# Performance work log

Hardware: AMD Instinct MI355X
Metric: run time of the kernel (lower is better)

## Reference

```python
import jax, jax.numpy as jnp
import numpy as np

EPS = 1e-12

def _natural_vvg_sym(x):
    """Natural vector visibility graph for one example.
    x: [S, D]. Returns symmetric 0/1 adjacency [S, S] = vg + vg.T (vg upper-triangular).
    Node a sees node b (a<b) iff for all a<c<b:
        y_c < y_b + (y_a - y_b) * (b - c) / (b - a),  y_k = <x_k, x_b> / ||x_b||
    """
    S = x.shape[0]
    t = jnp.arange(S, dtype=x.dtype)
    norms = jnp.maximum(jnp.linalg.norm(x, axis=-1), EPS)        # [S]
    Y = (x @ x.T) / norms[:, None]                                # Y[b,c] = <x_c,x_b>/||x_b||
    d = jnp.diagonal(Y)                                           # y_b = ||x_b||, [S]
    ta = t[:, None, None]   # a axis
    tb = t[None, :, None]   # b axis
    tc = t[None, None, :]   # c axis
    denom = jnp.where(tb != ta, tb - ta, jnp.ones((), x.dtype))   # avoid 0/0 on diagonal
    # visibility line at time c for pair (a,b): [S,S,S] indexed [a,b,c]
    line = d[None, :, None] + (Y.T[:, :, None] - d[None, :, None]) * (tb - tc) / denom
    between = (tc > ta) & (tc < tb)                               # strict interior points
    blocked = jnp.any((Y[None, :, :] >= line) & between, axis=-1) # [a,b]
    upper = t[None, :] > t[:, None]                               # b > a
    vg = (upper & ~blocked).astype(x.dtype)                       # upper-triangular adjacency
    return vg + vg.T


def setup_inputs() -> dict:
    key = jax.random.key(0)
    k1, k2 = jax.random.split(key)
    token_embs = jax.random.normal(k1, (8, 256, 768), dtype=jnp.float32)
    W = jax.random.normal(k2, (768, 4), dtype=jnp.float32)
    return {"token_embs": token_embs, "W": W}


def reference(token_embs, W):
    # vg_sym: [B, S, S]
    vg_sym = jax.vmap(_natural_vvg_sym)(token_embs)
    # torch: out[i] = multi_dot([vg, example, W])[0] == vg_sym[0] @ example @ W
    row0 = vg_sym[:, 0, :]                          # [B, S]
    h = jnp.einsum('bs,bsd->bd', row0, token_embs)  # [B, 768]
    logits = h @ W                                  # [B, n_class]
    return jax.nn.log_softmax(logits, axis=-1)
```

## Files before the change

kernel.cpp:

```cpp
#include <hip/hip_runtime.h>
#include <hip/hip_bf16.h>

constexpr int S  = 256;
constexpr int D  = 768;
constexpr int KQ = 8;
constexpr int KS = D / KQ;
constexpr int GROWS = KQ * S;

typedef _Float16 half8  __attribute__((ext_vector_type(8)));
typedef _Float16 half4v __attribute__((ext_vector_type(4)));
typedef float    f32x4  __attribute__((ext_vector_type(4)));

__device__ const int TI_MAP[10] = {0,1,1,2,2,2,3,3,3,3};
__device__ const int TJ_MAP[10] = {0,0,1,0,1,2,0,1,2,3};

__global__ __launch_bounds__(256) void gram_kernel(const float* __restrict__ X,
                                                   float* __restrict__ G) {
    const int ti    = TI_MAP[blockIdx.x];
    const int tj    = TJ_MAP[blockIdx.x];
    const int batch = blockIdx.y;
    const int kq    = blockIdx.z;

    const float* Xq = X + (size_t)batch * S * D + kq * KS;

    __shared__ _Float16 Ah[64][104], Al[64][104], Bh[64][104], Bl[64][104];

    const int t    = threadIdx.x;
    const int srow = t >> 2;
    const int sk   = (t & 3) * 24;

    const float* pa = Xq + (size_t)(ti * 64 + srow) * D + sk;
    const float* pb = Xq + (size_t)(tj * 64 + srow) * D + sk;

#pragma unroll
    for (int c = 0; c < 6; ++c) {
        const int ko = sk + c * 4;
        const float4 va = *(const float4*)(pa + c * 4);
        const float4 vb = *(const float4*)(pb + c * 4);
        half4v ha, la, hb, lb;
        ha.x = (_Float16)va.x; la.x = (_Float16)(va.x - (float)ha.x);
        ha.y = (_Float16)va.y; la.y = (_Float16)(va.y - (float)ha.y);
        ha.z = (_Float16)va.z; la.z = (_Float16)(va.z - (float)ha.z);
        ha.w = (_Float16)va.w; la.w = (_Float16)(va.w - (float)ha.w);
        hb.x = (_Float16)vb.x; lb.x = (_Float16)(vb.x - (float)hb.x);
        hb.y = (_Float16)vb.y; lb.y = (_Float16)(vb.y - (float)hb.y);
        hb.z = (_Float16)vb.z; lb.z = (_Float16)(vb.z - (float)hb.z);
        hb.w = (_Float16)vb.w; lb.w = (_Float16)(vb.w - (float)hb.w);
        *(half4v*)&Ah[srow][ko] = ha;
        *(half4v*)&Al[srow][ko] = la;
        *(half4v*)&Bh[srow][ko] = hb;
        *(half4v*)&Bl[srow][ko] = lb;
    }
    __syncthreads();

    const int lane = t & 63;
    const int w    = t >> 6;
    const int frow = lane & 15;
    const int fko  = (lane >> 4) * 8;

    f32x4 acc[4] = {};
#pragma unroll
    for (int ks = 0; ks < 3; ++ks) {
        const int k0 = ks * 32 + fko;
        const half8 ah = *(const half8*)&Ah[w * 16 + frow][k0];
        const half8 al = *(const half8*)&Al[w * 16 + frow][k0];
#pragma unroll
        for (int n = 0; n < 4; ++n) {
            const half8 bh = *(const half8*)&Bh[n * 16 + frow][k0];
            const half8 bl = *(const half8*)&Bl[n * 16 + frow][k0];
            acc[n] = __builtin_amdgcn_mfma_f32_16x16x32_f16(ah, bh, acc[n], 0, 0, 0);
            acc[n] = __builtin_amdgcn_mfma_f32_16x16x32_f16(ah, bl, acc[n], 0, 0, 0);
            acc[n] = __builtin_amdgcn_mfma_f32_16x16x32_f16(al, bh, acc[n], 0, 0, 0);
        }
    }

    float* gout = G + ((size_t)(batch * S + ti * 64 + w * 16 + (lane >> 4) * 4) * KQ + kq) * S
                    + tj * 64 + frow;
#pragma unroll
    for (int n = 0; n < 4; ++n)
#pragma unroll
        for (int r = 0; r < 4; ++r)
            gout[(size_t)r * GROWS + n * 16] = acc[n][r];
}

__global__ __launch_bounds__(256) void visxw_kernel(const float* __restrict__ X,
                                                    const float* __restrict__ Wm,
                                                    const float* __restrict__ G,
                                                    float* __restrict__ P,
                                                    float* __restrict__ wv) {
    const int batch = blockIdx.y;
    const int wave  = threadIdx.x >> 6;
    const int lane  = threadIdx.x & 63;
    const int b     = blockIdx.x * 4 + wave;

    const float* rbp = G + (size_t)(batch * S + b) * GROWS + 4 * lane;
    float4 s0 = make_float4(0.f, 0.f, 0.f, 0.f), s1 = s0, s2 = s0, s3 = s0;
    if (4 * lane <= b) {
#pragma unroll
        for (int sl = 0; sl < 2; ++sl) {
            const float4 v0 = *(const float4*)(rbp + (size_t)(4 * sl + 0) * S);
            const float4 v1 = *(const float4*)(rbp + (size_t)(4 * sl + 1) * S);
            const float4 v2 = *(const float4*)(rbp + (size_t)(4 * sl + 2) * S);
            const float4 v3 = *(const float4*)(rbp + (size_t)(4 * sl + 3) * S);
            s0.x += v0.x; s0.y += v0.y; s0.z += v0.z; s0.w += v0.w;
            s1.x += v1.x; s1.y += v1.y; s1.z += v1.z; s1.w += v1.w;
            s2.x += v2.x; s2.y += v2.y; s2.z += v2.z; s2.w += v2.w;
            s3.x += v3.x; s3.y += v3.y; s3.z += v3.z; s3.w += v3.w;
        }
    }
    float4 gs;
    gs.x = (s0.x + s1.x) + (s2.x + s3.x);
    gs.y = (s0.y + s1.y) + (s2.y + s3.y);
    gs.z = (s0.z + s1.z) + (s2.z + s3.z);
    gs.w = (s0.w + s1.w) + (s2.w + s3.w);

    const int bq = b & 3;
    float sel = (bq == 0) ? gs.x : ((bq == 1) ? gs.y : ((bq == 2) ? gs.z : gs.w));
    const float gb = __shfl(sel, b >> 2);
    const float g0 = __shfl(gs.x, 0);
    const float denom = (b > 0) ? (float)b : 1.0f;

    bool blocked = false;
    {
        const int c0 = 4 * lane;
#define VTEST(Q, GV) { const int c = c0 + (Q); \
        const float line = gb + ((g0 - gb) * (float)(b - c)) / denom; \
        if (c >= 1 && c < b && (GV) >= line) blocked = true; }
        VTEST(0, gs.x) VTEST(1, gs.y) VTEST(2, gs.z) VTEST(3, gs.w)
#undef VTEST
    }
    const bool visflag = (b >= 1) && !__any(blocked);

    const float* xs = X + ((size_t)batch * S + b) * D;
    float a0 = 0.f, a1 = 0.f, a2 = 0.f, a3 = 0.f;
#pragma unroll
    for (int i = 0; i < 3; ++i) {
        const int d0 = (lane + 64 * i) * 4;
        const float4 xv = *(const float4*)(xs + d0);
        const float xf[4] = {xv.x, xv.y, xv.z, xv.w};
#pragma unroll
        for (int j = 0; j < 4; ++j) {
            const float4 wq = *(const float4*)(Wm + (size_t)(d0 + j) * 4);
            a0 = fmaf(xf[j], wq.x, a0);
            a1 = fmaf(xf[j], wq.y, a1);
            a2 = fmaf(xf[j], wq.z, a2);
            a3 = fmaf(xf[j], wq.w, a3);
        }
    }
#pragma unroll
    for (int off = 32; off; off >>= 1) {
        a0 += __shfl_xor(a0, off);
        a1 += __shfl_xor(a1, off);
        a2 += __shfl_xor(a2, off);
        a3 += __shfl_xor(a3, off);
    }
    if (lane == 0) {
        float4 o = {a0, a1, a2, a3};
        *(float4*)(P + ((size_t)batch * S + b) * 4) = o;
        wv[batch * S + b] = visflag ? 1.0f : 0.0f;
    }
}

__global__ __launch_bounds__(256) void head_kernel(const float* __restrict__ P,
                                                   const float* __restrict__ wv,
                                                   float* __restrict__ out) {
    const int batch = blockIdx.x;
    const int k     = threadIdx.x >> 6;
    const int lane  = threadIdx.x & 63;

    float sum = 0.f;
#pragma unroll
    for (int i = 0; i < 4; ++i) {
        const int s = lane + 64 * i;
        sum = fmaf(wv[batch * S + s], P[((size_t)batch * S + s) * 4 + k], sum);
    }
#pragma unroll
    for (int off = 32; off; off >>= 1) sum += __shfl_xor(sum, off);

    __shared__ float lsh[4];
    if (lane == 0) lsh[k] = sum;
    __syncthreads();

    if (threadIdx.x == 0) {
        const float l0 = lsh[0], l1 = lsh[1], l2 = lsh[2], l3 = lsh[3];
        const float m = fmaxf(fmaxf(l0, l1), fmaxf(l2, l3));
        const float lse = logf(expf(l0 - m) + expf(l1 - m) + expf(l2 - m) + expf(l3 - m));
        out[batch * 4 + 0] = l0 - m - lse;
        out[batch * 4 + 1] = l1 - m - lse;
        out[batch * 4 + 2] = l2 - m - lse;
        out[batch * 4 + 3] = l3 - m - lse;
    }
}

extern "C" void kernel_launch(void* const* d_in, const int* in_sizes, int n_in,
                              void* d_out, int out_size, void* d_ws, size_t ws_size,
                              hipStream_t stream) {
    const float* X  = (const float*)d_in[0];
    const float* Wm = (const float*)d_in[1];
    float* out = (float*)d_out;

    float* ws = (float*)d_ws;
    float* P  = ws;
    float* wv = ws + 8192;
    float* G  = ws + 10240;

    gram_kernel <<<dim3(10, 8, 8), 256, 0, stream>>>(X, G);
    visxw_kernel<<<dim3(64, 8),    256, 0, stream>>>(X, Wm, G, P, wv);
    head_kernel <<<8,              256, 0, stream>>>(P, wv, out);
}
```

Measured before the change: 20.49 us.

## Fuse X·W projection into diagonal gram tiles and skip redundant B staging

The per-token X·W projection moves out of the visibility kernel and into the diagonal gram-kernel blocks, which already hold their X slice in registers. Each diagonal block writes per-k-slice partial projections, and the head kernel sums them only for visible tokens. Diagonal tiles also stop loading and splitting the B operand and reuse the A shared-memory tiles instead. This removes a second full read of X in the visibility kernel, at the cost of extra work and imbalance in the diagonal gram blocks and a larger partial-projection buffer.

```diff
diff --git a/kernel.cpp b/kernel.cpp
--- a/kernel.cpp
+++ b/kernel.cpp
@@ -15,43 +15,87 @@
 __device__ const int TJ_MAP[10] = {0,0,1,0,1,2,0,1,2,3};
 
 __global__ __launch_bounds__(256) void gram_kernel(const float* __restrict__ X,
-                                                   float* __restrict__ G) {
+                                                   const float* __restrict__ Wm,
+                                                   float* __restrict__ G,
+                                                   float* __restrict__ Ppart) {
     const int ti    = TI_MAP[blockIdx.x];
     const int tj    = TJ_MAP[blockIdx.x];
     const int batch = blockIdx.y;
     const int kq    = blockIdx.z;
+    const bool diag = (ti == tj);
 
     const float* Xq = X + (size_t)batch * S * D + kq * KS;
 
-    __shared__ _Float16 Ah[64][104], Al[64][104], Bh[64][104], Bl[64][104];
+    __shared__ _Float16 AhS[64][104], AlS[64][104], BhS[64][104], BlS[64][104];
+    __shared__ float Ws[96][4];
 
     const int t    = threadIdx.x;
     const int srow = t >> 2;
     const int sk   = (t & 3) * 24;
 
+    if (diag && t < 96)
+        *(float4*)&Ws[t][0] = *(const float4*)(Wm + (size_t)(kq * KS + t) * 4);
+
     const float* pa = Xq + (size_t)(ti * 64 + srow) * D + sk;
     const float* pb = Xq + (size_t)(tj * 64 + srow) * D + sk;
 
+    float4 xva[6];
 #pragma unroll
     for (int c = 0; c < 6; ++c) {
         const int ko = sk + c * 4;
         const float4 va = *(const float4*)(pa + c * 4);
-        const float4 vb = *(const float4*)(pb + c * 4);
-        half4v ha, la, hb, lb;
+        xva[c] = va;
+        half4v ha, la;
         ha.x = (_Float16)va.x; la.x = (_Float16)(va.x - (float)ha.x);
         ha.y = (_Float16)va.y; la.y = (_Float16)(va.y - (float)ha.y);
         ha.z = (_Float16)va.z; la.z = (_Float16)(va.z - (float)ha.z);
         ha.w = (_Float16)va.w; la.w = (_Float16)(va.w - (float)ha.w);
-        hb.x = (_Float16)vb.x; lb.x = (_Float16)(vb.x - (float)hb.x);
-        hb.y = (_Float16)vb.y; lb.y = (_Float16)(vb.y - (float)hb.y);
-        hb.z = (_Float16)vb.z; lb.z = (_Float16)(vb.z - (float)hb.z);
-        hb.w = (_Float16)vb.w; lb.w = (_Float16)(vb.w - (float)hb.w);
-        *(half4v*)&Ah[srow][ko] = ha;
-        *(half4v*)&Al[srow][ko] = la;
-        *(half4v*)&Bh[srow][ko] = hb;
-        *(half4v*)&Bl[srow][ko] = lb;
+        *(half4v*)&AhS[srow][ko] = ha;
+        *(half4v*)&AlS[srow][ko] = la;
+    }
+    if (!diag) {
+#pragma unroll
+        for (int c = 0; c < 6; ++c) {
+            const int ko = sk + c * 4;
+            const float4 vb = *(const float4*)(pb + c * 4);
+            half4v hb, lb;
+            hb.x = (_Float16)vb.x; lb.x = (_Float16)(vb.x - (float)hb.x);
+            hb.y = (_Float16)vb.y; lb.y = (_Float16)(vb.y - (float)hb.y);
+            hb.z = (_Float16)vb.z; lb.z = (_Float16)(vb.z - (float)hb.z);
+            hb.w = (_Float16)vb.w; lb.w = (_Float16)(vb.w - (float)hb.w);
+            *(half4v*)&BhS[srow][ko] = hb;
+            *(half4v*)&BlS[srow][ko] = lb;
+        }
     }
     __syncthreads();
+
+    if (diag) {
+        float4 pacc = make_float4(0.f, 0.f, 0.f, 0.f);
+#pragma unroll
+        for (int c = 0; c < 6; ++c) {
+            const float xf[4] = {xva[c].x, xva[c].y, xva[c].z, xva[c].w};
+#pragma unroll
+            for (int q = 0; q < 4; ++q) {
+                const float4 wq = *(const float4*)&Ws[sk + c * 4 + q][0];
+                pacc.x = fmaf(xf[q], wq.x, pacc.x);
+                pacc.y = fmaf(xf[q], wq.y, pacc.y);
+                pacc.z = fmaf(xf[q], wq.z, pacc.z);
+                pacc.w = fmaf(xf[q], wq.w, pacc.w);
+            }
+        }
+#pragma unroll
+        for (int off = 1; off <= 2; off <<= 1) {
+            pacc.x += __shfl_xor(pacc.x, off);
+            pacc.y += __shfl_xor(pacc.y, off);
+            pacc.z += __shfl_xor(pacc.z, off);
+            pacc.w += __shfl_xor(pacc.w, off);
+        }
+        if ((t & 3) == 0)
+            *(float4*)(Ppart + (((size_t)batch * S + ti * 64 + srow) * KQ + kq) * 4) = pacc;
+    }
+
+    _Float16 (*Bh)[104] = diag ? AhS : BhS;
+    _Float16 (*Bl)[104] = diag ? AlS : BlS;
 
     const int lane = t & 63;
     const int w    = t >> 6;
@@ -62,8 +106,8 @@
 #pragma unroll
     for (int ks = 0; ks < 3; ++ks) {
         const int k0 = ks * 32 + fko;
-        const half8 ah = *(const half8*)&Ah[w * 16 + frow][k0];
-        const half8 al = *(const half8*)&Al[w * 16 + frow][k0];
+        const half8 ah = *(const half8*)&AhS[w * 16 + frow][k0];
+        const half8 al = *(const half8*)&AlS[w * 16 + frow][k0];
 #pragma unroll
         for (int n = 0; n < 4; ++n) {
             const half8 bh = *(const half8*)&Bh[n * 16 + frow][k0];
@@ -83,11 +127,8 @@
             gout[(size_t)r * GROWS + n * 16] = acc[n][r];
 }
 
-__global__ __launch_bounds__(256) void visxw_kernel(const float* __restrict__ X,
-                                                    const float* __restrict__ Wm,
-                                                    const float* __restrict__ G,
-                                                    float* __restrict__ P,
-                                                    float* __restrict__ wv) {
+__global__ __launch_bounds__(256) void vis_kernel(const float* __restrict__ G,
+                                                  float* __restrict__ wv) {
     const int batch = blockIdx.y;
     const int wave  = threadIdx.x >> 6;
     const int lane  = threadIdx.x & 63;
@@ -131,58 +172,43 @@
     }
     const bool visflag = (b >= 1) && !__any(blocked);
 
-    const float* xs = X + ((size_t)batch * S + b) * D;
-    float a0 = 0.f, a1 = 0.f, a2 = 0.f, a3 = 0.f;
-#pragma unroll
-    for (int i = 0; i < 3; ++i) {
-        const int d0 = (lane + 64 * i) * 4;
-        const float4 xv = *(const float4*)(xs + d0);
-        const float xf[4] = {xv.x, xv.y, xv.z, xv.w};
-#pragma unroll
-        for (int j = 0; j < 4; ++j) {
-            const float4 wq = *(const float4*)(Wm + (size_t)(d0 + j) * 4);
-            a0 = fmaf(xf[j], wq.x, a0);
-            a1 = fmaf(xf[j], wq.y, a1);
-            a2 = fmaf(xf[j], wq.z, a2);
-            a3 = fmaf(xf[j], wq.w, a3);
-        }
-    }
-#pragma unroll
-    for (int off = 32; off; off >>= 1) {
-        a0 += __shfl_xor(a0, off);
-        a1 += __shfl_xor(a1, off);
-        a2 += __shfl_xor(a2, off);
-        a3 += __shfl_xor(a3, off);
-    }
-    if (lane == 0) {
-        float4 o = {a0, a1, a2, a3};
-        *(float4*)(P + ((size_t)batch * S + b) * 4) = o;
-        wv[batch * S + b] = visflag ? 1.0f : 0.0f;
-    }
-}
-
-__global__ __launch_bounds__(256) void head_kernel(const float* __restrict__ P,
+    if (lane == 0) wv[batch * S + b] = visflag ? 1.0f : 0.0f;
+}
+
+__global__ __launch_bounds__(256) void head_kernel(const float* __restrict__ Ppart,
                                                    const float* __restrict__ wv,
                                                    float* __restrict__ out) {
     const int batch = blockIdx.x;
-    const int k     = threadIdx.x >> 6;
-    const int lane  = threadIdx.x & 63;
-
-    float sum = 0.f;
-#pragma unroll
-    for (int i = 0; i < 4; ++i) {
-        const int s = lane + 64 * i;
-        sum = fmaf(wv[batch * S + s], P[((size_t)batch * S + s) * 4 + k], sum);
-    }
-#pragma unroll
-    for (int off = 32; off; off >>= 1) sum += __shfl_xor(sum, off);
-
-    __shared__ float lsh[4];
-    if (lane == 0) lsh[k] = sum;
+    const int t     = threadIdx.x;
+    const int wave  = t >> 6;
+    const int lane  = t & 63;
+
+    float4 acc = make_float4(0.f, 0.f, 0.f, 0.f);
+    if (wv[batch * S + t] != 0.0f) {
+        const float* pp = Ppart + ((size_t)batch * S + t) * (KQ * 4);
+#pragma unroll
+        for (int kq = 0; kq < KQ; ++kq) {
+            const float4 p = *(const float4*)(pp + kq * 4);
+            acc.x += p.x; acc.y += p.y; acc.z += p.z; acc.w += p.w;
+        }
+    }
+#pragma unroll
+    for (int off = 32; off; off >>= 1) {
+        acc.x += __shfl_xor(acc.x, off);
+        acc.y += __shfl_xor(acc.y, off);
+        acc.z += __shfl_xor(acc.z, off);
+        acc.w += __shfl_xor(acc.w, off);
+    }
+
+    __shared__ float4 lsh[4];
+    if (lane == 0) lsh[wave] = acc;
     __syncthreads();
 
-    if (threadIdx.x == 0) {
-        const float l0 = lsh[0], l1 = lsh[1], l2 = lsh[2], l3 = lsh[3];
+    if (t == 0) {
+        const float l0 = ((lsh[0].x + lsh[1].x) + (lsh[2].x + lsh[3].x));
+        const float l1 = ((lsh[0].y + lsh[1].y) + (lsh[2].y + lsh[3].y));
+        const float l2 = ((lsh[0].z + lsh[1].z) + (lsh[2].z + lsh[3].z));
+        const float l3 = ((lsh[0].w + lsh[1].w) + (lsh[2].w + lsh[3].w));
         const float m = fmaxf(fmaxf(l0, l1), fmaxf(l2, l3));
         const float lse = logf(expf(l0 - m) + expf(l1 - m) + expf(l2 - m) + expf(l3 - m));
         out[batch * 4 + 0] = l0 - m - lse;
@@ -200,11 +226,11 @@
     float* out = (float*)d_out;
 
     float* ws = (float*)d_ws;
-    float* P  = ws;
-    float* wv = ws + 8192;
-    float* G  = ws + 10240;
-
-    gram_kernel <<<dim3(10, 8, 8), 256, 0, stream>>>(X, G);
-    visxw_kernel<<<dim3(64, 8),    256, 0, stream>>>(X, Wm, G, P, wv);
-    head_kernel <<<8,              256, 0, stream>>>(P, wv, out);
-}
+    float* Ppart = ws;
+    float* wv    = ws + 65536;
+    float* G     = ws + 65536 + 2048;
+
+    gram_kernel<<<dim3(10, 8, 8), 256, 0, stream>>>(X, Wm, G, Ppart);
+    vis_kernel <<<dim3(64, 8),    256, 0, stream>>>(G, wv);
+    head_kernel<<<8,              256, 0, stream>>>(Ppart, wv, out);
+}
```

Measured after the change: 19.69 us. -3.9%, faster.
